# Kernel tuning notes

Hardware: AMD Instinct MI355X
Metric: run time of the kernel (lower is better)

## Reference

```python
import jax, jax.numpy as jnp
import numpy as np

EPS_PROJ = 0.004   # float32 branch of _project
EPS_MIN = 1e-15


def _poincare_linear(x, weight_v, weight_g, bias, c):
    c = c.reshape(())
    rc = jnp.sqrt(c)
    # z_unit: column-normalized weight (weight_v / ||weight_v||_col)
    z_unit = weight_v / jnp.maximum(jnp.linalg.norm(weight_v, axis=0), EPS_MIN)  # [in, out]
    # unidirectional Poincare MLR
    drcr = 2.0 * rc * bias                                  # [out]
    rcx = rc * x                                            # [N, in]
    cx2 = jnp.sum(rcx * rcx, axis=-1, keepdims=True)        # [N, 1]
    num = 2.0 * (rcx @ z_unit) * jnp.cosh(drcr) - (1.0 + cx2) * jnp.sinh(drcr)
    mlr = 2.0 * weight_g / rc * jnp.arcsinh(num / jnp.maximum(1.0 - cx2, EPS_MIN))  # [N, out]
    # map back to the ball: sinh, then gyro-half map
    y = jnp.sinh(rc * mlr) / rc
    y = y / (1.0 + jnp.sqrt(1.0 + c * jnp.sum(y * y, axis=-1, keepdims=True)))
    # _project onto ball of curvature k = -c
    k = -c
    maxnorm = (1.0 - EPS_PROJ) / jnp.sqrt(jnp.maximum(jnp.abs(k), EPS_MIN))
    maxnorm = jnp.where(k < 0, maxnorm, jnp.float32(1e15))
    norm = jnp.maximum(jnp.linalg.norm(y, axis=-1, keepdims=True), EPS_MIN)
    return jnp.where(norm > maxnorm, y / norm * maxnorm, y)


def setup_inputs() -> dict:
    key = jax.random.key(0)
    k1, k2, k3 = jax.random.split(key, 3)
    N, IN, OUT = 32768, 1024, 1024
    # points strictly inside the unit Poincare ball (||x|| ~ 0.64)
    x = jax.random.normal(k1, (N, IN), dtype=jnp.float32) * 0.02
    std = (2.0 * IN * OUT) ** (-0.5)
    weight_v = jax.random.normal(k2, (IN, OUT), dtype=jnp.float32) * std
    weight_g = jax.random.uniform(k3, (OUT,), dtype=jnp.float32, minval=0.5, maxval=1.5) * std * (IN ** 0.5)
    bias = jnp.zeros((OUT,), dtype=jnp.float32)
    c = jnp.ones((1,), dtype=jnp.float32)
    return {"x": x, "weight_v": weight_v, "weight_g": weight_g, "bias": bias, "c": c}


def reference(x, weight_v, weight_g, bias, c):
    return _poincare_linear(x, weight_v, weight_g, bias, c)
```

## Files before the change

### kernel.cpp

```cpp
#include <hip/hip_runtime.h>

#define K_DIM 1024
#define N_DIM 1024

typedef short v8s __attribute__((ext_vector_type(8)));
typedef float v4f __attribute__((ext_vector_type(4)));

__device__ __forceinline__ unsigned int bf16_rne(float f) {
    unsigned int u = __float_as_uint(f);
    u += 0x7FFFu + ((u >> 16) & 1u);
    return u >> 16;
}

__global__ void sumsq_cols(const float* __restrict__ wv, float* __restrict__ colss) {
    __shared__ float red[4][64];
    const int t = threadIdx.x;
    const int cj = t & 63, rr = t >> 6;
    const int col = (blockIdx.x & 15) * 64 + cj;
    const int k0 = (blockIdx.x >> 4) * 128 + rr * 32;
    float ss = 0.f;
#pragma unroll 8
    for (int i = 0; i < 32; ++i) {
        float v = wv[(size_t)(k0 + i) * N_DIM + col];
        ss = fmaf(v, v, ss);
    }
    red[rr][cj] = ss;
    __syncthreads();
    if (rr == 0) atomicAdd(&colss[col], red[0][cj] + red[1][cj] + red[2][cj] + red[3][cj]);
}

__global__ void finalize_cols(const float* __restrict__ colss, const float* __restrict__ wg,
                              const float* __restrict__ bias, const float* __restrict__ cptr,
                              float* __restrict__ colinv, float* __restrict__ coshd,
                              float* __restrict__ sinhd, float* __restrict__ gfac) {
    const int col = blockIdx.x * 256 + threadIdx.x;
    const float rc = sqrtf(cptr[0]);
    colinv[col] = 1.0f / fmaxf(sqrtf(colss[col]), 1e-15f);
    float d = 2.0f * rc * bias[col];
    float e = __expf(d), ie = 1.0f / e;
    coshd[col] = 0.5f * (e + ie);
    sinhd[col] = 0.5f * (e - ie);
    gfac[col] = 2.0f * wg[col];
}

__global__ void build_bt(const float* __restrict__ wv, const float* __restrict__ colinv,
                         unsigned short* __restrict__ Btf) {
    __shared__ float tile[64 * 65];
    const int t = threadIdx.x;
    const int ti = blockIdx.x & 15;
    const int tj = blockIdx.x >> 4;
    {
        const int kl = t >> 2;
        const int cc = t & 3;
        const float* src = wv + (size_t)(ti * 64 + kl) * N_DIM + tj * 64 + cc * 16;
        float4 fq[4];
#pragma unroll
        for (int i = 0; i < 4; ++i) fq[i] = ((const float4*)src)[i];
        float* dst = &tile[kl * 65 + cc * 16];
#pragma unroll
        for (int i = 0; i < 4; ++i) {
            dst[4 * i + 0] = fq[i].x; dst[4 * i + 1] = fq[i].y;
            dst[4 * i + 2] = fq[i].z; dst[4 * i + 3] = fq[i].w;
        }
    }
    __syncthreads();
    {
        const int nl = t & 63, kc = t >> 6;
        const int n = tj * 64 + nl;
        const float ci = colinv[n];
        const int nt_g = tj * 4 + (nl >> 4);
#pragma unroll
        for (int h = 0; h < 2; ++h) {
            const int k8g = ti * 8 + kc * 2 + h;
            const int ks_g = k8g >> 2;
            const int L = (nl & 15) | ((k8g & 3) << 4);
            unsigned int p[4];
#pragma unroll
            for (int j = 0; j < 4; ++j) {
                float v0 = tile[(kc * 16 + h * 8 + 2 * j) * 65 + nl] * ci;
                float v1 = tile[(kc * 16 + h * 8 + 2 * j + 1) * 65 + nl] * ci;
                p[j] = bf16_rne(v0) | (bf16_rne(v1) << 16);
            }
            *(uint4*)(Btf + ((size_t)(nt_g * 32 + ks_g) * 64 + L) * 8) =
                make_uint4(p[0], p[1], p[2], p[3]);
        }
    }
}

__launch_bounds__(256, 3)
__global__ void gemm_phase(const float* __restrict__ x, const unsigned short* __restrict__ Btf,
                           const float* __restrict__ cptr, const float* __restrict__ coshd,
                           const float* __restrict__ sinhd, const float* __restrict__ gfac,
                           float* __restrict__ out, float* __restrict__ rowsum) {
    __shared__ __align__(16) unsigned short As[16 * 512];
    __shared__ __align__(16) unsigned short Bs[16 * 512];
    __shared__ float s_cx2[128];
    __shared__ float s_rsum[128];

    const int t = threadIdx.x;
    const int w = t >> 6, L = t & 63;
    const int lm = L & 15, q = L >> 4;
    const int bn = blockIdx.x & 7;
    const int bm = blockIdx.x >> 3;
    const int r0 = bm * 128;

    if (t < 128) { s_cx2[t] = 0.f; s_rsum[t] = 0.f; }

    v4f acc[16];
#pragma unroll
    for (int i = 0; i < 16; ++i) acc[i] = (v4f){0.f, 0.f, 0.f, 0.f};

    const int smt0 = w * 2;
    const float* xr0 = x + (size_t)(r0 + smt0 * 16 + lm) * K_DIM;
    const float* xr1 = xr0 + (size_t)16 * K_DIM;
    float xp0 = 0.f, xp1 = 0.f;
    const int wm = w & 1, wn = w >> 1;

    for (int kq = 0; kq < 16; ++kq) {
        const int kbase = kq * 64;
#pragma unroll
        for (int i = 0; i < 4; ++i) {
            const int nt = smt0 + (i & 1);
            const int ks = i >> 1;
            const unsigned short* gp =
                Btf + ((size_t)((bn * 8 + nt) * 32 + (kq * 2 + ks)) * 64 + L) * 8;
            __builtin_amdgcn_global_load_lds(
                (const __attribute__((address_space(1))) unsigned int*)gp,
                (__attribute__((address_space(3))) unsigned int*)&Bs[(nt * 2 + ks) * 512],
                16, 0, 0);
        }
#pragma unroll
        for (int i = 0; i < 4; ++i) {
            const int half = i & 1;
            const int ks = i >> 1;
            const float* xr = half ? xr1 : xr0;
            const int kg = kbase + ks * 32 + q * 8;
            float4 f0 = *(const float4*)(xr + kg);
            float4 f1 = *(const float4*)(xr + kg + 4);
            float vals[8] = {f0.x, f0.y, f0.z, f0.w, f1.x, f1.y, f1.z, f1.w};
            unsigned int pk[4];
            float ssl = 0.f;
#pragma unroll
            for (int j = 0; j < 4; ++j) {
                ssl = fmaf(vals[2 * j], vals[2 * j], ssl);
                ssl = fmaf(vals[2 * j + 1], vals[2 * j + 1], ssl);
                pk[j] = bf16_rne(vals[2 * j]) | (bf16_rne(vals[2 * j + 1]) << 16);
            }
            if (half) xp1 += ssl; else xp0 += ssl;
            *(uint4*)&As[((smt0 + half) * 2 + ks) * 512 + L * 8] =
                make_uint4(pk[0], pk[1], pk[2], pk[3]);
        }
        __syncthreads();
#pragma unroll
        for (int ks = 0; ks < 2; ++ks) {
            v8s a[4], b[4];
#pragma unroll
            for (int mi = 0; mi < 4; ++mi)
                a[mi] = *(const v8s*)&As[((wm * 4 + mi) * 2 + ks) * 512 + L * 8];
#pragma unroll
            for (int ni = 0; ni < 4; ++ni)
                b[ni] = *(const v8s*)&Bs[((wn * 4 + ni) * 2 + ks) * 512 + L * 8];
#pragma unroll
            for (int mi = 0; mi < 4; ++mi)
#pragma unroll
                for (int ni = 0; ni < 4; ++ni)
                    acc[mi * 4 + ni] = __builtin_amdgcn_mfma_f32_16x16x32_bf16(
                        a[mi], b[ni], acc[mi * 4 + ni], 0, 0, 0);
        }
        __syncthreads();
    }

    atomicAdd(&s_cx2[smt0 * 16 + lm], xp0);
    atomicAdd(&s_cx2[smt0 * 16 + 16 + lm], xp1);
    __syncthreads();

    const float cc = cptr[0];
    const float rc = sqrtf(cc);
    const float two_rc = 2.0f * rc;
    const float halfinvrc = 0.5f / rc;
    float ch[4], sh[4], gf[4];
#pragma unroll
    for (int ni = 0; ni < 4; ++ni) {
        const int n = bn * 128 + wn * 64 + ni * 16 + lm;
        ch[ni] = coshd[n]; sh[ni] = sinhd[n]; gf[ni] = gfac[n];
    }
#pragma unroll
    for (int mi = 0; mi < 4; ++mi) {
        const int mloc = wm * 64 + mi * 16 + q * 4;
        float sx[4];
#pragma unroll
        for (int rr = 0; rr < 4; ++rr) sx[rr] = cc * s_cx2[mloc + rr];
        float rs[4] = {0.f, 0.f, 0.f, 0.f};
#pragma unroll
        for (int ni = 0; ni < 4; ++ni) {
            v4f d = acc[mi * 4 + ni];
#pragma unroll
            for (int rr = 0; rr < 4; ++rr) {
                float cx2 = sx[rr];
                float num = two_rc * d[rr] * ch[ni] - (1.0f + cx2) * sh[ni];
                float den = fmaxf(1.0f - cx2, 1e-15f);
                float tt = num * __builtin_amdgcn_rcpf(den);
                float as_ = __logf(fabsf(tt) + sqrtf(fmaf(tt, tt, 1.0f)));
                as_ = copysignf(as_, tt);
                float u = gf[ni] * as_;
                float e = __expf(u);
                float y = (e - __builtin_amdgcn_rcpf(e)) * halfinvrc;
                d[rr] = y;
                rs[rr] = fmaf(y, y, rs[rr]);
            }
            acc[mi * 4 + ni] = d;
        }
#pragma unroll
        for (int rr = 0; rr < 4; ++rr) {
            float v = rs[rr];
            v += __shfl_xor(v, 1); v += __shfl_xor(v, 2);
            v += __shfl_xor(v, 4); v += __shfl_xor(v, 8);
            if (lm == 0) atomicAdd(&s_rsum[mloc + rr], v);
        }
#pragma unroll
        for (int rr = 0; rr < 4; ++rr) {
            const int row = r0 + mloc + rr;
            float* op = out + (size_t)row * N_DIM + bn * 128 + wn * 64 + lm;
#pragma unroll
            for (int ni = 0; ni < 4; ++ni) op[ni * 16] = acc[mi * 4 + ni][rr];
        }
    }
    __syncthreads();
    if (t < 128) atomicAdd(&rowsum[r0 + t], s_rsum[t]);
}

__global__ void rescale(float* __restrict__ out, const float* __restrict__ rowsum,
                        const float* __restrict__ cptr) {
    const int row = blockIdx.x;
    const float cc = cptr[0];
    const float s = rowsum[row];
    const float scale = 1.0f / (1.0f + sqrtf(fmaf(cc, s, 1.0f)));
    const float nrm = fmaxf(sqrtf(s) * scale, 1e-15f);
    const float mn = (cc > 0.f) ? 0.996f / sqrtf(fmaxf(cc, 1e-15f)) : 1e15f;
    const float f = scale * (nrm > mn ? mn / nrm : 1.0f);
    float4* p = (float4*)(out + (size_t)row * N_DIM) + threadIdx.x;
    float4 v = *p;
    v.x *= f; v.y *= f; v.z *= f; v.w *= f;
    *p = v;
}

extern "C" void kernel_launch(void* const* d_in, const int* in_sizes, int n_in,
                              void* d_out, int out_size, void* d_ws, size_t ws_size,
                              hipStream_t stream) {
    const float* x    = (const float*)d_in[0];
    const float* wv   = (const float*)d_in[1];
    const float* wg   = (const float*)d_in[2];
    const float* bias = (const float*)d_in[3];
    const float* cptr = (const float*)d_in[4];
    float* out = (float*)d_out;

    const int OUT = in_sizes[2];
    const int IN  = in_sizes[1] / OUT;
    const int M   = in_sizes[0] / IN;

    float* colss  = (float*)d_ws;
    float* rowsum = colss + 1024;
    float* colinv = rowsum + M;
    float* coshd  = colinv + 1024;
    float* sinhd  = coshd + 1024;
    float* gfac   = sinhd + 1024;
    unsigned short* Btf = (unsigned short*)(gfac + 1024);

    hipMemsetAsync(colss, 0, (size_t)(1024 + M) * sizeof(float), stream);
    sumsq_cols<<<128, 256, 0, stream>>>(wv, colss);
    finalize_cols<<<OUT / 256, 256, 0, stream>>>(colss, wg, bias, cptr, colinv, coshd, sinhd, gfac);
    build_bt<<<(IN / 64) * (OUT / 64), 256, 0, stream>>>(wv, colinv, Btf);
    gemm_phase<<<(M / 128) * (OUT / 128), 256, 0, stream>>>(x, Btf, cptr, coshd, sinhd, gfac, out, rowsum);
    rescale<<<M, 256, 0, stream>>>(out, rowsum, cptr);
}
```

Measured before the change: 426.6 us.

## Pre-convert activations to bf16 MFMA layout before GEMM and load via LDS DMA

Adds a prep_a kernel that converts x to bf16 once, writes it in the MFMA fragment layout and computes row sums of squares. A new gemm_fast kernel loads both operands through global_load_lds and no longer re-reads and re-converts fp32 x for each of the 8 column blocks. It also raises occupancy to 4 blocks per CU. This adds a separate pass over x (a 64MB fp32 read plus a 64MB bf16 write) and needs extra workspace, falling back to the old path when the workspace is too small. The rescale kernel now handles 4 rows per block.

```diff
diff --git a/kernel.cpp b/kernel.cpp
--- a/kernel.cpp
+++ b/kernel.cpp
@@ -87,11 +87,56 @@
     }
 }
 
-__launch_bounds__(256, 3)
-__global__ void gemm_phase(const float* __restrict__ x, const unsigned short* __restrict__ Btf,
-                           const float* __restrict__ cptr, const float* __restrict__ coshd,
-                           const float* __restrict__ sinhd, const float* __restrict__ gfac,
-                           float* __restrict__ out, float* __restrict__ rowsum) {
+__global__ void prep_a(const float* __restrict__ x, unsigned short* __restrict__ Axf,
+                       float* __restrict__ rowss) {
+    __shared__ float xs[16 * 1028];
+    const int t = threadIdx.x;
+    const int b = blockIdx.x;
+    {
+        const int r = t >> 4;
+        const int c = t & 15;
+        const float* xp = x + (size_t)(b * 16 + r) * K_DIM + c * 4;
+        float* dst = &xs[r * 1028 + c * 4];
+        float ss = 0.f;
+#pragma unroll
+        for (int it = 0; it < 16; ++it) {
+            float4 v = *(const float4*)(xp + it * 64);
+            ss = fmaf(v.x, v.x, ss); ss = fmaf(v.y, v.y, ss);
+            ss = fmaf(v.z, v.z, ss); ss = fmaf(v.w, v.w, ss);
+            *(float4*)(dst + it * 64) = v;
+        }
+        ss += __shfl_xor(ss, 1); ss += __shfl_xor(ss, 2);
+        ss += __shfl_xor(ss, 4); ss += __shfl_xor(ss, 8);
+        if (c == 0) rowss[b * 16 + r] = ss;
+    }
+    __syncthreads();
+    {
+        const int w = t >> 6, L = t & 63;
+        const int lm = L & 15, q = L >> 4;
+#pragma unroll
+        for (int i = 0; i < 8; ++i) {
+            const int ks = w * 8 + i;
+            const float* src = &xs[lm * 1028 + ks * 32 + q * 8];
+            float4 f0 = *(const float4*)(src);
+            float4 f1 = *(const float4*)(src + 4);
+            float vals[8] = {f0.x, f0.y, f0.z, f0.w, f1.x, f1.y, f1.z, f1.w};
+            unsigned int p[4];
+#pragma unroll
+            for (int j = 0; j < 4; ++j)
+                p[j] = bf16_rne(vals[2 * j]) | (bf16_rne(vals[2 * j + 1]) << 16);
+            *(uint4*)(Axf + ((size_t)b * 32 + ks) * 512 + L * 8) =
+                make_uint4(p[0], p[1], p[2], p[3]);
+        }
+    }
+}
+
+__launch_bounds__(256, 4)
+__global__ void gemm_fast(const unsigned short* __restrict__ Axf,
+                          const unsigned short* __restrict__ Btf,
+                          const float* __restrict__ rowss, const float* __restrict__ cptr,
+                          const float* __restrict__ coshd, const float* __restrict__ sinhd,
+                          const float* __restrict__ gfac,
+                          float* __restrict__ out, float* __restrict__ rowsum) {
     __shared__ __align__(16) unsigned short As[16 * 512];
     __shared__ __align__(16) unsigned short Bs[16 * 512];
     __shared__ float s_cx2[128];
@@ -104,52 +149,38 @@
     const int bm = blockIdx.x >> 3;
     const int r0 = bm * 128;
 
-    if (t < 128) { s_cx2[t] = 0.f; s_rsum[t] = 0.f; }
+    if (t < 128) { s_cx2[t] = rowss[r0 + t]; s_rsum[t] = 0.f; }
 
     v4f acc[16];
 #pragma unroll
     for (int i = 0; i < 16; ++i) acc[i] = (v4f){0.f, 0.f, 0.f, 0.f};
 
-    const int smt0 = w * 2;
-    const float* xr0 = x + (size_t)(r0 + smt0 * 16 + lm) * K_DIM;
-    const float* xr1 = xr0 + (size_t)16 * K_DIM;
-    float xp0 = 0.f, xp1 = 0.f;
+    const int mt0 = w * 2;
     const int wm = w & 1, wn = w >> 1;
 
     for (int kq = 0; kq < 16; ++kq) {
-        const int kbase = kq * 64;
 #pragma unroll
         for (int i = 0; i < 4; ++i) {
-            const int nt = smt0 + (i & 1);
+            const int mtl = mt0 + (i & 1);
             const int ks = i >> 1;
             const unsigned short* gp =
-                Btf + ((size_t)((bn * 8 + nt) * 32 + (kq * 2 + ks)) * 64 + L) * 8;
+                Axf + ((size_t)((bm * 8 + mtl) * 32) + (kq * 2 + ks)) * 512 + L * 8;
+            __builtin_amdgcn_global_load_lds(
+                (const __attribute__((address_space(1))) unsigned int*)gp,
+                (__attribute__((address_space(3))) unsigned int*)&As[(mtl * 2 + ks) * 512],
+                16, 0, 0);
+        }
+#pragma unroll
+        for (int i = 0; i < 4; ++i) {
+            const int nt = mt0 + (i & 1);
+            const int ks = i >> 1;
+            const unsigned short* gp =
+                Btf + ((size_t)((bn * 8 + nt) * 32) + (kq * 2 + ks)) * 512 + L * 8;
             __builtin_amdgcn_global_load_lds(
                 (const __attribute__((address_space(1))) unsigned int*)gp,
                 (__attribute__((address_space(3))) unsigned int*)&Bs[(nt * 2 + ks) * 512],
                 16, 0, 0);
         }
-#pragma unroll
-        for (int i = 0; i < 4; ++i) {
-            const int half = i & 1;
-            const int ks = i >> 1;
-            const float* xr = half ? xr1 : xr0;
-            const int kg = kbase + ks * 32 + q * 8;
-            float4 f0 = *(const float4*)(xr + kg);
-            float4 f1 = *(const float4*)(xr + kg + 4);
-            float vals[8] = {f0.x, f0.y, f0.z, f0.w, f1.x, f1.y, f1.z, f1.w};
-            unsigned int pk[4];
-            float ssl = 0.f;
-#pragma unroll
-            for (int j = 0; j < 4; ++j) {
-                ssl = fmaf(vals[2 * j], vals[2 * j], ssl);
-                ssl = fmaf(vals[2 * j + 1], vals[2 * j + 1], ssl);
-                pk[j] = bf16_rne(vals[2 * j]) | (bf16_rne(vals[2 * j + 1]) << 16);
-            }
-            if (half) xp1 += ssl; else xp0 += ssl;
-            *(uint4*)&As[((smt0 + half) * 2 + ks) * 512 + L * 8] =
-                make_uint4(pk[0], pk[1], pk[2], pk[3]);
-        }
         __syncthreads();
 #pragma unroll
         for (int ks = 0; ks < 2; ++ks) {
@@ -169,10 +200,6 @@
         }
         __syncthreads();
     }
-
-    atomicAdd(&s_cx2[smt0 * 16 + lm], xp0);
-    atomicAdd(&s_cx2[smt0 * 16 + 16 + lm], xp1);
-    __syncthreads();
 
     const float cc = cptr[0];
     const float rc = sqrtf(cc);
@@ -229,19 +256,165 @@
     if (t < 128) atomicAdd(&rowsum[r0 + t], s_rsum[t]);
 }
 
+__launch_bounds__(256, 3)
+__global__ void gemm_phase(const float* __restrict__ x, const unsigned short* __restrict__ Btf,
+                           const float* __restrict__ cptr, const float* __restrict__ coshd,
+                           const float* __restrict__ sinhd, const float* __restrict__ gfac,
+                           float* __restrict__ out, float* __restrict__ rowsum) {
+    __shared__ __align__(16) unsigned short As[16 * 512];
+    __shared__ __align__(16) unsigned short Bs[16 * 512];
+    __shared__ float s_cx2[128];
+    __shared__ float s_rsum[128];
+
+    const int t = threadIdx.x;
+    const int w = t >> 6, L = t & 63;
+    const int lm = L & 15, q = L >> 4;
+    const int bn = blockIdx.x & 7;
+    const int bm = blockIdx.x >> 3;
+    const int r0 = bm * 128;
+
+    if (t < 128) { s_cx2[t] = 0.f; s_rsum[t] = 0.f; }
+
+    v4f acc[16];
+#pragma unroll
+    for (int i = 0; i < 16; ++i) acc[i] = (v4f){0.f, 0.f, 0.f, 0.f};
+
+    const int smt0 = w * 2;
+    const float* xr0 = x + (size_t)(r0 + smt0 * 16 + lm) * K_DIM;
+    const float* xr1 = xr0 + (size_t)16 * K_DIM;
+    float xp0 = 0.f, xp1 = 0.f;
+    const int wm = w & 1, wn = w >> 1;
+
+    for (int kq = 0; kq < 16; ++kq) {
+        const int kbase = kq * 64;
+#pragma unroll
+        for (int i = 0; i < 4; ++i) {
+            const int nt = smt0 + (i & 1);
+            const int ks = i >> 1;
+            const unsigned short* gp =
+                Btf + ((size_t)((bn * 8 + nt) * 32 + (kq * 2 + ks)) * 64 + L) * 8;
+            __builtin_amdgcn_global_load_lds(
+                (const __attribute__((address_space(1))) unsigned int*)gp,
+                (__attribute__((address_space(3))) unsigned int*)&Bs[(nt * 2 + ks) * 512],
+                16, 0, 0);
+        }
+#pragma unroll
+        for (int i = 0; i < 4; ++i) {
+            const int half = i & 1;
+            const int ks = i >> 1;
+            const float* xr = half ? xr1 : xr0;
+            const int kg = kbase + ks * 32 + q * 8;
+            float4 f0 = *(const float4*)(xr + kg);
+            float4 f1 = *(const float4*)(xr + kg + 4);
+            float vals[8] = {f0.x, f0.y, f0.z, f0.w, f1.x, f1.y, f1.z, f1.w};
+            unsigned int pk[4];
+            float ssl = 0.f;
+#pragma unroll
+            for (int j = 0; j < 4; ++j) {
+                ssl = fmaf(vals[2 * j], vals[2 * j], ssl);
+                ssl = fmaf(vals[2 * j + 1], vals[2 * j + 1], ssl);
+                pk[j] = bf16_rne(vals[2 * j]) | (bf16_rne(vals[2 * j + 1]) << 16);
+            }
+            if (half) xp1 += ssl; else xp0 += ssl;
+            *(uint4*)&As[((smt0 + half) * 2 + ks) * 512 + L * 8] =
+                make_uint4(pk[0], pk[1], pk[2], pk[3]);
+        }
+        __syncthreads();
+#pragma unroll
+        for (int ks = 0; ks < 2; ++ks) {
+            v8s a[4], b[4];
+#pragma unroll
+            for (int mi = 0; mi < 4; ++mi)
+                a[mi] = *(const v8s*)&As[((wm * 4 + mi) * 2 + ks) * 512 + L * 8];
+#pragma unroll
+            for (int ni = 0; ni < 4; ++ni)
+                b[ni] = *(const v8s*)&Bs[((wn * 4 + ni) * 2 + ks) * 512 + L * 8];
+#pragma unroll
+            for (int mi = 0; mi < 4; ++mi)
+#pragma unroll
+                for (int ni = 0; ni < 4; ++ni)
+                    acc[mi * 4 + ni] = __builtin_amdgcn_mfma_f32_16x16x32_bf16(
+                        a[mi], b[ni], acc[mi * 4 + ni], 0, 0, 0);
+        }
+        __syncthreads();
+    }
+
+    atomicAdd(&s_cx2[smt0 * 16 + lm], xp0);
+    atomicAdd(&s_cx2[smt0 * 16 + 16 + lm], xp1);
+    __syncthreads();
+
+    const float cc = cptr[0];
+    const float rc = sqrtf(cc);
+    const float two_rc = 2.0f * rc;
+    const float halfinvrc = 0.5f / rc;
+    float ch[4], sh[4], gf[4];
+#pragma unroll
+    for (int ni = 0; ni < 4; ++ni) {
+        const int n = bn * 128 + wn * 64 + ni * 16 + lm;
+        ch[ni] = coshd[n]; sh[ni] = sinhd[n]; gf[ni] = gfac[n];
+    }
+#pragma unroll
+    for (int mi = 0; mi < 4; ++mi) {
+        const int mloc = wm * 64 + mi * 16 + q * 4;
+        float sx[4];
+#pragma unroll
+        for (int rr = 0; rr < 4; ++rr) sx[rr] = cc * s_cx2[mloc + rr];
+        float rs[4] = {0.f, 0.f, 0.f, 0.f};
+#pragma unroll
+        for (int ni = 0; ni < 4; ++ni) {
+            v4f d = acc[mi * 4 + ni];
+#pragma unroll
+            for (int rr = 0; rr < 4; ++rr) {
+                float cx2 = sx[rr];
+                float num = two_rc * d[rr] * ch[ni] - (1.0f + cx2) * sh[ni];
+                float den = fmaxf(1.0f - cx2, 1e-15f);
+                float tt = num * __builtin_amdgcn_rcpf(den);
+                float as_ = __logf(fabsf(tt) + sqrtf(fmaf(tt, tt, 1.0f)));
+                as_ = copysignf(as_, tt);
+                float u = gf[ni] * as_;
+                float e = __expf(u);
+                float y = (e - __builtin_amdgcn_rcpf(e)) * halfinvrc;
+                d[rr] = y;
+                rs[rr] = fmaf(y, y, rs[rr]);
+            }
+            acc[mi * 4 + ni] = d;
+        }
+#pragma unroll
+        for (int rr = 0; rr < 4; ++rr) {
+            float v = rs[rr];
+            v += __shfl_xor(v, 1); v += __shfl_xor(v, 2);
+            v += __shfl_xor(v, 4); v += __shfl_xor(v, 8);
+            if (lm == 0) atomicAdd(&s_rsum[mloc + rr], v);
+        }
+#pragma unroll
+        for (int rr = 0; rr < 4; ++rr) {
+            const int row = r0 + mloc + rr;
+            float* op = out + (size_t)row * N_DIM + bn * 128 + wn * 64 + lm;
+#pragma unroll
+            for (int ni = 0; ni < 4; ++ni) op[ni * 16] = acc[mi * 4 + ni][rr];
+        }
+    }
+    __syncthreads();
+    if (t < 128) atomicAdd(&rowsum[r0 + t], s_rsum[t]);
+}
+
 __global__ void rescale(float* __restrict__ out, const float* __restrict__ rowsum,
                         const float* __restrict__ cptr) {
-    const int row = blockIdx.x;
+    const int t = threadIdx.x;
+    const int row = blockIdx.x * 4 + (t >> 6);
     const float cc = cptr[0];
     const float s = rowsum[row];
     const float scale = 1.0f / (1.0f + sqrtf(fmaf(cc, s, 1.0f)));
     const float nrm = fmaxf(sqrtf(s) * scale, 1e-15f);
     const float mn = (cc > 0.f) ? 0.996f / sqrtf(fmaxf(cc, 1e-15f)) : 1e15f;
     const float f = scale * (nrm > mn ? mn / nrm : 1.0f);
-    float4* p = (float4*)(out + (size_t)row * N_DIM) + threadIdx.x;
-    float4 v = *p;
-    v.x *= f; v.y *= f; v.z *= f; v.w *= f;
-    *p = v;
+    float4* p = (float4*)(out + (size_t)row * N_DIM) + (t & 63);
+#pragma unroll
+    for (int j = 0; j < 4; ++j) {
+        float4 v = p[j * 64];
+        v.x *= f; v.y *= f; v.z *= f; v.w *= f;
+        p[j * 64] = v;
+    }
 }
 
 extern "C" void kernel_launch(void* const* d_in, const int* in_sizes, int n_in,
@@ -260,16 +433,29 @@
 
     float* colss  = (float*)d_ws;
     float* rowsum = colss + 1024;
-    float* colinv = rowsum + M;
+    float* rowss  = rowsum + M;
+    float* colinv = rowss + M;
     float* coshd  = colinv + 1024;
     float* sinhd  = coshd + 1024;
     float* gfac   = sinhd + 1024;
     unsigned short* Btf = (unsigned short*)(gfac + 1024);
-
-    hipMemsetAsync(colss, 0, (size_t)(1024 + M) * sizeof(float), stream);
+    unsigned short* Axf = Btf + (size_t)IN * OUT;
+
+    const size_t need = (size_t)(1024 + 2 * M + 4096) * 4 + (size_t)IN * OUT * 2
+                      + (size_t)M * IN * 2;
+
+    hipMemsetAsync(rowsum, 0, (size_t)M * sizeof(float), stream);
+    hipMemsetAsync(colss, 0, 1024 * sizeof(float), stream);
     sumsq_cols<<<128, 256, 0, stream>>>(wv, colss);
     finalize_cols<<<OUT / 256, 256, 0, stream>>>(colss, wg, bias, cptr, colinv, coshd, sinhd, gfac);
     build_bt<<<(IN / 64) * (OUT / 64), 256, 0, stream>>>(wv, colinv, Btf);
-    gemm_phase<<<(M / 128) * (OUT / 128), 256, 0, stream>>>(x, Btf, cptr, coshd, sinhd, gfac, out, rowsum);
-    rescale<<<M, 256, 0, stream>>>(out, rowsum, cptr);
-}
+    if (ws_size >= need) {
+        prep_a<<<M / 16, 256, 0, stream>>>(x, Axf, rowss);
+        gemm_fast<<<(M / 128) * (OUT / 128), 256, 0, stream>>>(
+            Axf, Btf, rowss, cptr, coshd, sinhd, gfac, out, rowsum);
+    } else {
+        gemm_phase<<<(M / 128) * (OUT / 128), 256, 0, stream>>>(
+            x, Btf, cptr, coshd, sinhd, gfac, out, rowsum);
+    }
+    rescale<<<M / 4, 256, 0, stream>>>(out, rowsum, cptr);
+}
```

Result: faster. 397.4 us (-6.9%).
